# Optimization experiments

Measured on AMD Instinct MI355X. Metric: run time of the kernel, lower is better.

## Reference

```python
import jax, jax.numpy as jnp
import numpy as np

BERT_DIM = 1024
HIDDEN = 64          # GlobalPointer head size d
NUM_TYPE = 9
MASK_NEG = 1.0e12


def _rope_sin_cos(seq_len, dim, dtype=jnp.float32):
    # sinusoidal_position_embedding: emb[s, 2i]=sin(s*w_i), emb[s,2i+1]=cos(s*w_i)
    pos = jnp.arange(seq_len, dtype=dtype)[:, None]                  # [S,1]
    inv = jnp.power(10000.0, -2.0 * jnp.arange(dim // 2, dtype=dtype) / dim)
    ang = pos * inv                                                   # [S,D/2]
    sin_pos = jnp.repeat(jnp.sin(ang), 2, axis=-1)                    # [S,D] = emb[..., ::2] interleave-2
    cos_pos = jnp.repeat(jnp.cos(ang), 2, axis=-1)                    # [S,D] = emb[..., 1::2] interleave-2
    return sin_pos, cos_pos


def _rotate(x):
    # stack([-x[...,1::2], x[...,::2]], -1).reshape(x.shape)
    x2 = jnp.stack([-x[..., 1::2], x[..., ::2]], axis=-1)
    return x2.reshape(x.shape)


def setup_inputs() -> dict:
    key = jax.random.key(0)
    k1, k2, k3 = jax.random.split(key, 3)
    B, S = 16, 512
    hidden = jax.random.normal(k1, (B, S, BERT_DIM), dtype=jnp.float32)
    attention_mask = jnp.ones((B, S), dtype=jnp.float32)
    W = jax.random.normal(k2, (BERT_DIM, NUM_TYPE * HIDDEN * 2), dtype=jnp.float32) * (1.0 / np.sqrt(BERT_DIM))
    b = jax.random.normal(k3, (NUM_TYPE * HIDDEN * 2,), dtype=jnp.float32) * 0.02
    return {"bert_last_hidden_state": hidden, "attention_mask": attention_mask, "W": W, "b": b}


def reference(bert_last_hidden_state, attention_mask, W, b):
    h = bert_last_hidden_state                                        # [B,S,bert_dim]
    B, S, _ = h.shape
    out = h @ W + b                                                   # [B,S,T*2d]
    # split into T chunks of 2d and stack on dim -2 == reshape
    out = out.reshape(B, S, NUM_TYPE, 2 * HIDDEN)
    qw, kw = out[..., :HIDDEN], out[..., HIDDEN:]                     # [B,S,T,d]
    sin_pos, cos_pos = _rope_sin_cos(S, HIDDEN, h.dtype)              # [S,d]
    sin_pos = sin_pos[None, :, None, :]                               # [1,S,1,d]
    cos_pos = cos_pos[None, :, None, :]
    qw = qw * cos_pos + _rotate(qw) * sin_pos
    kw = kw * cos_pos + _rotate(kw) * sin_pos
    logits = jnp.einsum('bmhd,bnhd->bhmn', qw, kw)                    # [B,T,S,S]
    pad = attention_mask[:, None, None, :]                            # [B,1,1,S] -> broadcast [B,T,S,S]
    logits = logits * pad - (1.0 - pad) * MASK_NEG
    return logits / jnp.sqrt(jnp.asarray(HIDDEN, logits.dtype))
```

## Files before the change

### kernel.cpp

```cpp
#include <hip/hip_runtime.h>
#include <hip/hip_bf16.h>

#define BDIM 1024
#define NCOL 1152
#define HEADS 9
#define HID 64
#define SLEN 512
#define BATCH 16

typedef __attribute__((ext_vector_type(8))) short bf16x8;
typedef __attribute__((ext_vector_type(8))) unsigned short u16x8;
typedef __attribute__((ext_vector_type(4))) float f32x4;
typedef __attribute__((ext_vector_type(4))) unsigned short u16x4;

static __device__ __forceinline__ unsigned short f2bf(float f) {
    union { float f; unsigned int u; } x; x.f = f;
    unsigned int u = x.u;
    unsigned int r = (u + 0x7fffu + ((u >> 16) & 1u)) >> 16;
    return (unsigned short)r;
}

#define GLOAD_LDS16(g, l)                                                     \
    __builtin_amdgcn_global_load_lds(                                         \
        (const __attribute__((address_space(1))) unsigned int*)(g),           \
        (__attribute__((address_space(3))) unsigned int*)(l), 16, 0, 0)

__global__ __launch_bounds__(256) void prep_kernel(const float* __restrict__ hidden,
                                                   const float* __restrict__ W,
                                                   unsigned short* __restrict__ Ab,
                                                   unsigned short* __restrict__ Wt,
                                                   float* __restrict__ sctab) {
    __shared__ float tile[32][33];
    const int b = blockIdx.x;
    if (b < 4096) {
        int i = (b * 256 + threadIdx.x) * 8;
        float4 a = *reinterpret_cast<const float4*>(hidden + i);
        float4 c = *reinterpret_cast<const float4*>(hidden + i + 4);
        u16x8 p;
        p[0] = f2bf(a.x); p[1] = f2bf(a.y); p[2] = f2bf(a.z); p[3] = f2bf(a.w);
        p[4] = f2bf(c.x); p[5] = f2bf(c.y); p[6] = f2bf(c.z); p[7] = f2bf(c.w);
        *reinterpret_cast<u16x8*>(Ab + i) = p;
    } else if (b < 5248) {
        const int bb = b - 4096;
        const int tx = threadIdx.x & 31;
        const int ty = threadIdx.x >> 5;
        const int nb = (bb % 36) * 32;
        const int kb = (bb / 36) * 32;
#pragma unroll
        for (int i = 0; i < 4; ++i) {
            int k = kb + ty + i * 8;
            tile[ty + i * 8][tx] = W[(size_t)k * NCOL + nb + tx];
        }
        __syncthreads();
#pragma unroll
        for (int i = 0; i < 4; ++i) {
            int n = nb + ty + i * 8;
            Wt[(size_t)n * BDIM + kb + tx] = f2bf(tile[tx][ty + i * 8]);
        }
    } else {
        int idx = (b - 5248) * 256 + threadIdx.x;
        int s = idx >> 5, j = idx & 31;
        float inv = powf(10000.0f, -(float)(2 * j) / (float)HID);
        float ang = (float)s * inv;
        sctab[idx * 2]     = sinf(ang);
        sctab[idx * 2 + 1] = cosf(ang);
    }
}

__global__ __launch_bounds__(512) void proj_rope_kernel(
    const unsigned short* __restrict__ Ab,
    const unsigned short* __restrict__ Wt,
    const float* __restrict__ bias,
    const float4* __restrict__ sctab4,
    unsigned short* __restrict__ qk)
{
    __shared__ __attribute__((aligned(16))) unsigned short As[3][256 * 64];
    __shared__ __attribute__((aligned(16))) unsigned short Bs[3][144 * 64];

    const int t = threadIdx.x;
    const int m0 = blockIdx.x * 256;
    const int n0 = blockIdx.y * 144;
    const int wid = t >> 6, lane = t & 63;
    const int lrow = lane & 15;
    const int lk = lane >> 4;

    const int rowoff = lane >> 3;
    const int sslot = (lane & 7) ^ rowoff;
    const unsigned short* gA = Ab + (size_t)(m0 + wid * 32 + rowoff) * BDIM + sslot * 8;
    const unsigned short* gB = Wt + (size_t)(n0 + wid * 24 + rowoff) * BDIM + sslot * 8;
    const int lA = wid * 2048;
    const int lB = wid * 1536;
    const bool hasB = (wid < 6);

#define STAGE_A(buf, k0)                                                      \
    do {                                                                      \
        GLOAD_LDS16(gA + (k0),             &As[buf][lA]);                     \
        GLOAD_LDS16(gA + (k0) + 8 * BDIM,  &As[buf][lA + 512]);               \
        GLOAD_LDS16(gA + (k0) + 16 * BDIM, &As[buf][lA + 1024]);              \
        GLOAD_LDS16(gA + (k0) + 24 * BDIM, &As[buf][lA + 1536]);              \
    } while (0)
#define STAGE_B(buf, k0)                                                      \
    do {                                                                      \
        GLOAD_LDS16(gB + (k0),             &Bs[buf][lB]);                     \
        GLOAD_LDS16(gB + (k0) + 8 * BDIM,  &Bs[buf][lB + 512]);               \
        GLOAD_LDS16(gB + (k0) + 16 * BDIM, &Bs[buf][lB + 1024]);              \
    } while (0)

    const int rkey = lrow & 7;

    f32x4 acc[9][2] = {};

    STAGE_A(0, 0);  if (hasB) STAGE_B(0, 0);
    STAGE_A(1, 64); if (hasB) STAGE_B(1, 64);

    int cur = 0;
    for (int it = 0; it < 16; ++it) {
        if (it < 15) {
            if (hasB) asm volatile("s_waitcnt vmcnt(7)" ::: "memory");
            else      asm volatile("s_waitcnt vmcnt(4)" ::: "memory");
        } else {
            asm volatile("s_waitcnt vmcnt(0)" ::: "memory");
        }
        __builtin_amdgcn_s_barrier();
        __builtin_amdgcn_sched_barrier(0);

        const char* Ac = (const char*)As[cur];
        const char* Bc = (const char*)Bs[cur];
        const int nb2 = (cur + 2 >= 3) ? cur - 1 : cur + 2;

        {
            const int fslot = (lk ^ rkey) << 4;
            bf16x8 af[2], bfr[9];
#pragma unroll
            for (int mi = 0; mi < 2; ++mi)
                af[mi] = *reinterpret_cast<const bf16x8*>(
                    Ac + (wid * 32 + mi * 16 + lrow) * 128 + fslot);
#pragma unroll
            for (int ni = 0; ni < 9; ++ni)
                bfr[ni] = *reinterpret_cast<const bf16x8*>(
                    Bc + (ni * 16 + lrow) * 128 + fslot);
            if (it < 14) STAGE_A(nb2, (it + 2) * 64);
            __builtin_amdgcn_sched_barrier(0);
            asm volatile("s_waitcnt lgkmcnt(0)" ::: "memory");
            __builtin_amdgcn_sched_barrier(0);
            __builtin_amdgcn_s_setprio(1);
#pragma unroll
            for (int ni = 0; ni < 9; ++ni)
#pragma unroll
                for (int mi = 0; mi < 2; ++mi)
                    acc[ni][mi] = __builtin_amdgcn_mfma_f32_16x16x32_bf16(
                        bfr[ni], af[mi], acc[ni][mi], 0, 0, 0);
            __builtin_amdgcn_s_setprio(0);
        }
        __builtin_amdgcn_s_barrier();
        __builtin_amdgcn_sched_barrier(0);

        {
            const int fslot = ((4 + lk) ^ rkey) << 4;
            bf16x8 af[2], bfr[9];
#pragma unroll
            for (int mi = 0; mi < 2; ++mi)
                af[mi] = *reinterpret_cast<const bf16x8*>(
                    Ac + (wid * 32 + mi * 16 + lrow) * 128 + fslot);
#pragma unroll
            for (int ni = 0; ni < 9; ++ni)
                bfr[ni] = *reinterpret_cast<const bf16x8*>(
                    Bc + (ni * 16 + lrow) * 128 + fslot);
            if (it < 14 && hasB) STAGE_B(nb2, (it + 2) * 64);
            __builtin_amdgcn_sched_barrier(0);
            asm volatile("s_waitcnt lgkmcnt(0)" ::: "memory");
            __builtin_amdgcn_sched_barrier(0);
            __builtin_amdgcn_s_setprio(1);
#pragma unroll
            for (int ni = 0; ni < 9; ++ni)
#pragma unroll
                for (int mi = 0; mi < 2; ++mi)
                    acc[ni][mi] = __builtin_amdgcn_mfma_f32_16x16x32_bf16(
                        bfr[ni], af[mi], acc[ni][mi], 0, 0, 0);
            __builtin_amdgcn_s_setprio(0);
        }

        cur = (cur + 1 >= 3) ? 0 : cur + 1;
    }
#undef STAGE_A
#undef STAGE_B

    const float4* bias4 = (const float4*)bias;
#pragma unroll
    for (int ni = 0; ni < 9; ++ni) {
        int cb = n0 + ni * 16 + lk * 4;
        float4 bv = bias4[cb >> 2];
        int h = cb >> 7;
        int qki = (cb >> 6) & 1;
        int d0 = cb & 63;
#pragma unroll
        for (int mi = 0; mi < 2; ++mi) {
            int m = m0 + wid * 32 + mi * 16 + lrow;
            int bi = m >> 9, s = m & 511;
            float4 sc = sctab4[s * 16 + (d0 >> 2)];
            f32x4 a = acc[ni][mi];
            float v0 = a[0] + bv.x, v1 = a[1] + bv.y;
            float v2 = a[2] + bv.z, v3 = a[3] + bv.w;
            u16x4 p;
            p[0] = f2bf(v0 * sc.y - v1 * sc.x);
            p[1] = f2bf(v1 * sc.y + v0 * sc.x);
            p[2] = f2bf(v2 * sc.w - v3 * sc.z);
            p[3] = f2bf(v3 * sc.w + v2 * sc.z);
            *reinterpret_cast<u16x4*>(
                qk + ((((size_t)bi * HEADS + h) * 2 + qki) * SLEN + s) * HID + d0) = p;
        }
    }
}

__global__ __launch_bounds__(256) void logits_kernel(
    const unsigned short* __restrict__ qkbuf,
    const float* __restrict__ mask,
    float* __restrict__ out)
{
    __shared__ __attribute__((aligned(16))) unsigned short Qs[128 * 72];
    __shared__ __attribute__((aligned(16))) unsigned short Ks[128 * 72];

    const int t = threadIdx.x;
    const int bz = blockIdx.z;
    const int bi = bz / 9;
    const int m0 = blockIdx.x * 128, n0 = blockIdx.y * 128;

    const unsigned short* Qg = qkbuf + ((size_t)bz * 2 + 0) * SLEN * HID + (size_t)m0 * HID;
    const unsigned short* Kg = qkbuf + ((size_t)bz * 2 + 1) * SLEN * HID + (size_t)n0 * HID;

#pragma unroll
    for (int i = 0; i < 4; ++i) {
        int e = t + i * 256;
        int row = e >> 3, c = e & 7;
        *reinterpret_cast<uint4*>(&Qs[row * 72 + c * 8]) =
            *reinterpret_cast<const uint4*>(Qg + (size_t)row * HID + c * 8);
        *reinterpret_cast<uint4*>(&Ks[row * 72 + c * 8]) =
            *reinterpret_cast<const uint4*>(Kg + (size_t)row * HID + c * 8);
    }
    __syncthreads();

    const int wid = t >> 6, lane = t & 63;
    const int wr = wid >> 1, wc = wid & 1;
    const int lrow = lane & 15;
    const int lk = lane >> 4;

    f32x4 acc[4][4] = {};
#pragma unroll
    for (int kk = 0; kk < 2; ++kk) {
        bf16x8 af[4], bfr[4];
#pragma unroll
        for (int mi = 0; mi < 4; ++mi)
            af[mi] = *reinterpret_cast<const bf16x8*>(
                &Qs[(wr * 64 + mi * 16 + lrow) * 72 + kk * 32 + lk * 8]);
#pragma unroll
        for (int ni = 0; ni < 4; ++ni)
            bfr[ni] = *reinterpret_cast<const bf16x8*>(
                &Ks[(wc * 64 + ni * 16 + lrow) * 72 + kk * 32 + lk * 8]);
#pragma unroll
        for (int ni = 0; ni < 4; ++ni)
#pragma unroll
            for (int mi = 0; mi < 4; ++mi)
                acc[ni][mi] = __builtin_amdgcn_mfma_f32_16x16x32_bf16(
                    bfr[ni], af[mi], acc[ni][mi], 0, 0, 0);
    }

    float4 pv[4]; float4 sub[4];
#pragma unroll
    for (int ni = 0; ni < 4; ++ni) {
        int nb = n0 + wc * 64 + ni * 16 + lk * 4;
        pv[ni] = *reinterpret_cast<const float4*>(mask + bi * SLEN + nb);
        sub[ni].x = (1.0f - pv[ni].x) * 1000000000000.0f;
        sub[ni].y = (1.0f - pv[ni].y) * 1000000000000.0f;
        sub[ni].z = (1.0f - pv[ni].z) * 1000000000000.0f;
        sub[ni].w = (1.0f - pv[ni].w) * 1000000000000.0f;
    }

    float* tr = reinterpret_cast<float*>(Qs);
    __syncthreads();
#pragma unroll
    for (int mi = 0; mi < 4; ++mi) {
        if (mi) __syncthreads();
#pragma unroll
        for (int ni = 0; ni < 4; ++ni) {
            int col = wc * 64 + ni * 16 + lk * 4;
            f32x4 a = acc[ni][mi];
            f32x4 o;
            o[0] = (a[0] * pv[ni].x - sub[ni].x) * 0.125f;
            o[1] = (a[1] * pv[ni].y - sub[ni].y) * 0.125f;
            o[2] = (a[2] * pv[ni].z - sub[ni].z) * 0.125f;
            o[3] = (a[3] * pv[ni].w - sub[ni].w) * 0.125f;
            *reinterpret_cast<f32x4*>(&tr[(wr * 16 + lrow) * 136 + col]) = o;
        }
        __syncthreads();
#pragma unroll
        for (int j = 0; j < 4; ++j) {
            int idx = t + j * 256;
            int r_l = idx >> 5, c4 = idx & 31;
            int m = m0 + (r_l >> 4) * 64 + mi * 16 + (r_l & 15);
            f32x4 v = *reinterpret_cast<const f32x4*>(&tr[r_l * 136 + c4 * 4]);
            *reinterpret_cast<f32x4*>(
                out + ((size_t)bz * SLEN + m) * SLEN + n0 + c4 * 4) = v;
        }
    }
}

extern "C" void kernel_launch(void* const* d_in, const int* in_sizes, int n_in,
                              void* d_out, int out_size, void* d_ws, size_t ws_size,
                              hipStream_t stream) {
    const float* hidden = (const float*)d_in[0];
    const float* mask   = (const float*)d_in[1];
    const float* W      = (const float*)d_in[2];
    const float* bias   = (const float*)d_in[3];
    float* out = (float*)d_out;

    char* ws = (char*)d_ws;
    unsigned short* Ab = (unsigned short*)ws;
    unsigned short* Wt = (unsigned short*)(ws + 16777216);
    float* sctab = (float*)(ws + 16777216 + 2359296);
    unsigned short* qk = (unsigned short*)(ws + 16777216 + 2359296 + 131072);

    prep_kernel<<<5312, 256, 0, stream>>>(hidden, W, Ab, Wt, sctab);
    proj_rope_kernel<<<dim3(32, 8), 512, 0, stream>>>(
        Ab, Wt, bias, (const float4*)sctab, qk);
    logits_kernel<<<dim3(4, 4, BATCH * HEADS), 256, 0, stream>>>(qk, mask, out);
}
```

Measured before the change: 73.24 us.

## Fuse hidden-state bf16 conversion into projection GEMM A-tile loading

Drops the separate prep pass that converted the fp32 hidden states to a bf16 workspace. The projection kernel now reads fp32 A directly into registers, converts with packed bf16 instructions, and writes swizzled tiles into a double-buffered LDS A stage. This removes a 32MB read plus 16MB write round trip. In exchange, each of the 8 column blocks rereads fp32 A (twice the bytes of bf16), and the register-staged prefetch is only one iteration deep instead of the previous async direct-to-LDS triple buffer.

```diff
diff --git a/kernel.cpp b/kernel.cpp
--- a/kernel.cpp
+++ b/kernel.cpp
@@ -20,32 +20,27 @@
     return (unsigned short)r;
 }
 
+static __device__ __forceinline__ unsigned int pk2bf(float lo, float hi) {
+    unsigned int r;
+    asm("v_cvt_pk_bf16_f32 %0, %1, %2" : "=v"(r) : "v"(lo), "v"(hi));
+    return r;
+}
+
 #define GLOAD_LDS16(g, l)                                                     \
     __builtin_amdgcn_global_load_lds(                                         \
         (const __attribute__((address_space(1))) unsigned int*)(g),           \
         (__attribute__((address_space(3))) unsigned int*)(l), 16, 0, 0)
 
-__global__ __launch_bounds__(256) void prep_kernel(const float* __restrict__ hidden,
-                                                   const float* __restrict__ W,
-                                                   unsigned short* __restrict__ Ab,
+__global__ __launch_bounds__(256) void prep_kernel(const float* __restrict__ W,
                                                    unsigned short* __restrict__ Wt,
                                                    float* __restrict__ sctab) {
     __shared__ float tile[32][33];
     const int b = blockIdx.x;
-    if (b < 4096) {
-        int i = (b * 256 + threadIdx.x) * 8;
-        float4 a = *reinterpret_cast<const float4*>(hidden + i);
-        float4 c = *reinterpret_cast<const float4*>(hidden + i + 4);
-        u16x8 p;
-        p[0] = f2bf(a.x); p[1] = f2bf(a.y); p[2] = f2bf(a.z); p[3] = f2bf(a.w);
-        p[4] = f2bf(c.x); p[5] = f2bf(c.y); p[6] = f2bf(c.z); p[7] = f2bf(c.w);
-        *reinterpret_cast<u16x8*>(Ab + i) = p;
-    } else if (b < 5248) {
-        const int bb = b - 4096;
+    if (b < 1152) {
         const int tx = threadIdx.x & 31;
         const int ty = threadIdx.x >> 5;
-        const int nb = (bb % 36) * 32;
-        const int kb = (bb / 36) * 32;
+        const int nb = (b % 36) * 32;
+        const int kb = (b / 36) * 32;
 #pragma unroll
         for (int i = 0; i < 4; ++i) {
             int k = kb + ty + i * 8;
@@ -58,7 +53,7 @@
             Wt[(size_t)n * BDIM + kb + tx] = f2bf(tile[tx][ty + i * 8]);
         }
     } else {
-        int idx = (b - 5248) * 256 + threadIdx.x;
+        int idx = (b - 1152) * 256 + threadIdx.x;
         int s = idx >> 5, j = idx & 31;
         float inv = powf(10000.0f, -(float)(2 * j) / (float)HID);
         float ang = (float)s * inv;
@@ -68,13 +63,13 @@
 }
 
 __global__ __launch_bounds__(512) void proj_rope_kernel(
-    const unsigned short* __restrict__ Ab,
+    const float* __restrict__ hidden,
     const unsigned short* __restrict__ Wt,
     const float* __restrict__ bias,
     const float4* __restrict__ sctab4,
     unsigned short* __restrict__ qk)
 {
-    __shared__ __attribute__((aligned(16))) unsigned short As[3][256 * 64];
+    __shared__ __attribute__((aligned(16))) unsigned short As[2][256 * 64];
     __shared__ __attribute__((aligned(16))) unsigned short Bs[3][144 * 64];
 
     const int t = threadIdx.x;
@@ -84,21 +79,16 @@
     const int lrow = lane & 15;
     const int lk = lane >> 4;
 
+    const int r8 = lane >> 4;
+    const int q  = lane & 15;
+    const float* aBase = hidden + (size_t)(m0 + wid * 32 + r8) * BDIM + q * 4;
+
     const int rowoff = lane >> 3;
     const int sslot = (lane & 7) ^ rowoff;
-    const unsigned short* gA = Ab + (size_t)(m0 + wid * 32 + rowoff) * BDIM + sslot * 8;
     const unsigned short* gB = Wt + (size_t)(n0 + wid * 24 + rowoff) * BDIM + sslot * 8;
-    const int lA = wid * 2048;
     const int lB = wid * 1536;
     const bool hasB = (wid < 6);
 
-#define STAGE_A(buf, k0)                                                      \
-    do {                                                                      \
-        GLOAD_LDS16(gA + (k0),             &As[buf][lA]);                     \
-        GLOAD_LDS16(gA + (k0) + 8 * BDIM,  &As[buf][lA + 512]);               \
-        GLOAD_LDS16(gA + (k0) + 16 * BDIM, &As[buf][lA + 1024]);              \
-        GLOAD_LDS16(gA + (k0) + 24 * BDIM, &As[buf][lA + 1536]);              \
-    } while (0)
 #define STAGE_B(buf, k0)                                                      \
     do {                                                                      \
         GLOAD_LDS16(gB + (k0),             &Bs[buf][lB]);                     \
@@ -106,27 +96,45 @@
         GLOAD_LDS16(gB + (k0) + 16 * BDIM, &Bs[buf][lB + 1024]);              \
     } while (0)
 
+#define LOAD_A(k0f)                                                           \
+    do {                                                                      \
+        _Pragma("unroll")                                                     \
+        for (int i = 0; i < 8; ++i)                                           \
+            av[i] = *reinterpret_cast<const f32x4*>(aBase + (k0f) + i * 4 * BDIM); \
+    } while (0)
+
+#define CVT_WRITE_A(buf)                                                      \
+    do {                                                                      \
+        _Pragma("unroll")                                                     \
+        for (int i = 0; i < 8; ++i) {                                         \
+            unsigned int lo_ = pk2bf(av[i][0], av[i][1]);                     \
+            unsigned int hi_ = pk2bf(av[i][2], av[i][3]);                     \
+            int rl_ = wid * 32 + i * 4 + r8;                                  \
+            int bo_ = (((q >> 1) ^ (rl_ & 7)) << 4) | ((q & 1) << 3);         \
+            *reinterpret_cast<uint2*>((char*)As[buf] + rl_ * 128 + bo_) =     \
+                make_uint2(lo_, hi_);                                         \
+        }                                                                     \
+    } while (0)
+
     const int rkey = lrow & 7;
 
     f32x4 acc[9][2] = {};
-
-    STAGE_A(0, 0);  if (hasB) STAGE_B(0, 0);
-    STAGE_A(1, 64); if (hasB) STAGE_B(1, 64);
-
-    int cur = 0;
+    f32x4 av[8];
+
+    LOAD_A(0);
+    if (hasB) { STAGE_B(0, 0); STAGE_B(1, 64); }
+    __builtin_amdgcn_sched_barrier(0);
+    CVT_WRITE_A(0);
+    asm volatile("s_waitcnt lgkmcnt(0)" ::: "memory");
+    if (hasB) asm volatile("s_waitcnt vmcnt(3)" ::: "memory");
+    __builtin_amdgcn_sched_barrier(0);
+
     for (int it = 0; it < 16; ++it) {
-        if (it < 15) {
-            if (hasB) asm volatile("s_waitcnt vmcnt(7)" ::: "memory");
-            else      asm volatile("s_waitcnt vmcnt(4)" ::: "memory");
-        } else {
-            asm volatile("s_waitcnt vmcnt(0)" ::: "memory");
-        }
         __builtin_amdgcn_s_barrier();
         __builtin_amdgcn_sched_barrier(0);
 
-        const char* Ac = (const char*)As[cur];
-        const char* Bc = (const char*)Bs[cur];
-        const int nb2 = (cur + 2 >= 3) ? cur - 1 : cur + 2;
+        const char* Ac = (const char*)As[it & 1];
+        const char* Bc = (const char*)Bs[it % 3];
 
         {
             const int fslot = (lk ^ rkey) << 4;
@@ -139,7 +147,7 @@
             for (int ni = 0; ni < 9; ++ni)
                 bfr[ni] = *reinterpret_cast<const bf16x8*>(
                     Bc + (ni * 16 + lrow) * 128 + fslot);
-            if (it < 14) STAGE_A(nb2, (it + 2) * 64);
+            if (it < 15) LOAD_A((it + 1) * 64);
             __builtin_amdgcn_sched_barrier(0);
             asm volatile("s_waitcnt lgkmcnt(0)" ::: "memory");
             __builtin_amdgcn_sched_barrier(0);
@@ -166,7 +174,7 @@
             for (int ni = 0; ni < 9; ++ni)
                 bfr[ni] = *reinterpret_cast<const bf16x8*>(
                     Bc + (ni * 16 + lrow) * 128 + fslot);
-            if (it < 14 && hasB) STAGE_B(nb2, (it + 2) * 64);
+            if (it < 14 && hasB) STAGE_B((it + 2) % 3, (it + 2) * 64);
             __builtin_amdgcn_sched_barrier(0);
             asm volatile("s_waitcnt lgkmcnt(0)" ::: "memory");
             __builtin_amdgcn_sched_barrier(0);
@@ -180,10 +188,15 @@
             __builtin_amdgcn_s_setprio(0);
         }
 
-        cur = (cur + 1 >= 3) ? 0 : cur + 1;
-    }
-#undef STAGE_A
+        if (it < 15) {
+            CVT_WRITE_A((it + 1) & 1);
+            asm volatile("s_waitcnt lgkmcnt(0)" ::: "memory");
+            __builtin_amdgcn_sched_barrier(0);
+        }
+    }
 #undef STAGE_B
+#undef LOAD_A
+#undef CVT_WRITE_A
 
     const float4* bias4 = (const float4*)bias;
 #pragma unroll
@@ -314,13 +327,12 @@
     float* out = (float*)d_out;
 
     char* ws = (char*)d_ws;
-    unsigned short* Ab = (unsigned short*)ws;
-    unsigned short* Wt = (unsigned short*)(ws + 16777216);
-    float* sctab = (float*)(ws + 16777216 + 2359296);
-    unsigned short* qk = (unsigned short*)(ws + 16777216 + 2359296 + 131072);
-
-    prep_kernel<<<5312, 256, 0, stream>>>(hidden, W, Ab, Wt, sctab);
+    unsigned short* Wt = (unsigned short*)ws;
+    float* sctab = (float*)(ws + 2359296);
+    unsigned short* qk = (unsigned short*)(ws + 2359296 + 131072);
+
+    prep_kernel<<<1216, 256, 0, stream>>>(W, Wt, sctab);
     proj_rope_kernel<<<dim3(32, 8), 512, 0, stream>>>(
-        Ab, Wt, bias, (const float4*)sctab, qk);
+        hidden, Wt, bias, (const float4*)sctab, qk);
     logits_kernel<<<dim3(4, 4, BATCH * HEADS), 256, 0, stream>>>(qk, mask, out);
 }
```

New measurement: 76.43 us. 1.04x slower.
